# Kernel tuning notes

Hardware: AMD Instinct MI355X
Metric: run time of the kernel (lower is better)

## Reference

```python
import jax, jax.numpy as jnp
import numpy as np
from jax import lax

KS = [3, 5, 7, 9]
DS = [1, 2, 3, 4]
BN_EPS = 1e-5


def setup_inputs() -> dict:
    key = jax.random.key(0)
    ks = jax.random.split(key, 16)
    B, Cin, H, W = 16, 64, 256, 256
    Ce = 64  # out_channels // 2
    inp = {"x": jax.random.normal(ks[0], (B, Cin, H, W), jnp.float32)}
    for i, (k, _) in enumerate(zip(KS, DS)):
        fan_in = Cin * k * k
        inp[f"w{i}"] = jax.random.normal(ks[1 + i], (Ce, Cin, k, k), jnp.float32) / np.sqrt(fan_in)
        inp[f"b{i}"] = jnp.zeros((Ce,), jnp.float32)
    inp["bn_scale"] = jnp.ones((4, Ce), jnp.float32)
    inp["bn_bias"] = jnp.zeros((4, Ce), jnp.float32)
    inp["bn_mean"] = jax.random.normal(ks[5], (4, Ce), jnp.float32) * 0.1
    inp["bn_var"] = jax.random.uniform(ks[6], (4, Ce), jnp.float32, 0.5, 1.5)
    inp["gate_w"] = jax.random.normal(ks[7], (4, Cin), jnp.float32) / np.sqrt(Cin)
    inp["gate_b"] = jnp.zeros((4,), jnp.float32)
    return inp


def _expert(x, w, b, scale, bias, mean, var, k, d):
    pad = d * (k - 1) // 2
    y = lax.conv_general_dilated(
        x, w, window_strides=(2, 2), padding=[(pad, pad), (pad, pad)],
        rhs_dilation=(d, d), dimension_numbers=("NCHW", "OIHW", "NCHW"))
    y = y + b[None, :, None, None]
    inv = scale * lax.rsqrt(var + BN_EPS)
    y = y * inv[None, :, None, None] + (bias - mean * inv)[None, :, None, None]
    return jax.nn.gelu(y, approximate=False)


def reference(x, w0, b0, w1, b1, w2, b2, w3, b3,
              bn_scale, bn_bias, bn_mean, bn_var, gate_w, gate_b):
    B = x.shape[0]
    # Gate: global average pool -> linear -> softmax -> top-2 renormalized
    pooled = x.mean(axis=(2, 3))                    # (B, Cin)
    gates = jax.nn.softmax(pooled @ gate_w.T + gate_b, axis=1)  # (B, 4)
    top2_w, top2_idx = lax.top_k(gates, 2)
    top2_w = top2_w / (top2_w.sum(axis=1, keepdims=True) + 1e-8)
    # Dense compute of all 4 experts (faithful to original module)
    ws, bs = [w0, w1, w2, w3], [b0, b1, b2, b3]
    outs = [
        _expert(x, ws[i], bs[i], bn_scale[i], bn_bias[i], bn_mean[i], bn_var[i], KS[i], DS[i])
        for i in range(4)
    ]
    E = jnp.stack(outs, axis=1)                     # (B, 4, Ce, H/2, W/2)
    sel = jnp.take_along_axis(E, top2_idx[:, :, None, None, None], axis=1)  # (B,2,Ce,h,w)
    weighted = sel * top2_w[:, :, None, None, None]
    # concat top-2 along channel dim == reshape (B,2,Ce,h,w) -> (B,2*Ce,h,w)
    Bc, two, Ce, h, w = weighted.shape
    return weighted.reshape(Bc, two * Ce, h, w)
```

## Files before the change

kernel.cpp:

```cpp
#include <hip/hip_runtime.h>
#include <hip/hip_bf16.h>
#include <math.h>

#define CIN 64
#define CE  64
#define HH  256
#define WW  256
#define OHW 128
#define PW  288
#define PH  288
#define WOFF 19600
#define TOFF (WOFF + 6144)

typedef __attribute__((ext_vector_type(8))) short bf16x8;
typedef __attribute__((ext_vector_type(4))) float f32x4;

static __device__ __forceinline__ unsigned short f2bf(float f) {
    __hip_bfloat16 h = __float2bfloat16(f);
    return *reinterpret_cast<unsigned short*>(&h);
}

#define GLOAD16(gsrc, ldst)                                                        \
    __builtin_amdgcn_global_load_lds(                                              \
        (const __attribute__((address_space(1))) void*)(gsrc),                     \
        (__attribute__((address_space(3))) void*)(ldst), 16, 0, 0)

template <bool PRE>
__global__ __launch_bounds__(256)
void poolcvt_kernel(const float* __restrict__ x, unsigned short* __restrict__ xbf,
                    float* __restrict__ partial) {
    int blk = blockIdx.x;
    int rc = blockIdx.y;
    int tid = threadIdx.x, lane = tid & 63, wv = tid >> 6;
    int c0 = lane * 4;
    const float* xb = x + (size_t)blk * 8 * (HH * WW);
    unsigned short* pl = xbf + (size_t)blk * (PW * PH) * 8;
    float s[8];
#pragma unroll
    for (int j = 0; j < 8; ++j) s[j] = 0.f;
#pragma unroll 1
    for (int rr = wv; rr < 32; rr += 4) {
        int h = rc * 32 + rr;
        float4 v[8];
#pragma unroll
        for (int j = 0; j < 8; ++j)
            v[j] = *reinterpret_cast<const float4*>(xb + (size_t)j * (HH * WW) + h * WW + c0);
#pragma unroll
        for (int j = 0; j < 8; ++j) s[j] += (v[j].x + v[j].y) + (v[j].z + v[j].w);
        if (PRE) {
            size_t o16 = ((size_t)(16 + h) * PW + 16 + c0);
            unsigned short u[4][8];
#pragma unroll
            for (int j = 0; j < 8; ++j) {
                u[0][j] = f2bf(v[j].x);
                u[1][j] = f2bf(v[j].y);
                u[2][j] = f2bf(v[j].z);
                u[3][j] = f2bf(v[j].w);
            }
#pragma unroll
            for (int cc = 0; cc < 4; ++cc)
                *reinterpret_cast<bf16x8*>(pl + (o16 + cc) * 8) =
                    *reinterpret_cast<const bf16x8*>(u[cc]);
        }
    }
    if (PRE) {
        bf16x8 z = (bf16x8)(short)0;
#pragma unroll 1
        for (int i = tid; i < 32 * 32; i += 256) {
            int rr = i >> 5, cc = i & 31;
            int pr = 16 + rc * 32 + rr;
            int pc = (cc < 16) ? cc : (256 + cc);
            *reinterpret_cast<bf16x8*>(pl + ((size_t)pr * PW + pc) * 8) = z;
        }
        if (rc == 0) {
#pragma unroll 1
            for (int i = tid; i < 16 * PW; i += 256)
                *reinterpret_cast<bf16x8*>(pl + (size_t)i * 8) = z;
        }
        if (rc == 7) {
#pragma unroll 1
            for (int i = tid; i < 16 * PW; i += 256)
                *reinterpret_cast<bf16x8*>(pl + ((size_t)(272 * PW) + i) * 8) = z;
        }
    }
#pragma unroll
    for (int j = 0; j < 8; ++j) {
#pragma unroll
        for (int m = 32; m >= 1; m >>= 1) s[j] += __shfl_xor(s[j], m, 64);
    }
    __shared__ float red[4][8];
    if (lane == 0) {
#pragma unroll
        for (int j = 0; j < 8; ++j) red[wv][j] = s[j];
    }
    __syncthreads();
    if (tid < 8) {
        int j = tid;
        float t = (red[0][j] + red[1][j]) + (red[2][j] + red[3][j]);
        partial[(blk * 8 + rc) * 8 + j] = t;
    }
}

__global__ __launch_bounds__(64)
void gate_kernel(const float* __restrict__ partial, const float* __restrict__ gw,
                 const float* __restrict__ gb, int* __restrict__ sel_idx,
                 float* __restrict__ sel_w) {
    int b = blockIdx.x;
    int c = threadIdx.x;
    float p = 0.f;
#pragma unroll
    for (int rc = 0; rc < 8; ++rc)
        p += partial[(((b * 8 + (c >> 3)) * 8) + rc) * 8 + (c & 7)];
    p *= (1.0f / (HH * WW));
    float l[4];
#pragma unroll
    for (int e = 0; e < 4; ++e) l[e] = p * gw[e * CIN + c];
#pragma unroll
    for (int m = 32; m >= 1; m >>= 1) {
#pragma unroll
        for (int e = 0; e < 4; ++e) l[e] += __shfl_xor(l[e], m, 64);
    }
    if (c == 0) {
        float g[4], s = 0.f;
#pragma unroll
        for (int e = 0; e < 4; ++e) l[e] += gb[e];
        float mx = fmaxf(fmaxf(l[0], l[1]), fmaxf(l[2], l[3]));
#pragma unroll
        for (int e = 0; e < 4; ++e) { g[e] = expf(l[e] - mx); s += g[e]; }
#pragma unroll
        for (int e = 0; e < 4; ++e) g[e] /= s;
        int i1 = 0;
        for (int e = 1; e < 4; ++e) if (g[e] > g[i1]) i1 = e;
        int i2 = -1;
        for (int e = 0; e < 4; ++e) {
            if (e == i1) continue;
            if (i2 < 0 || g[e] > g[i2]) i2 = e;
        }
        float den = g[i1] + g[i2] + 1e-8f;
        sel_idx[b * 2 + 0] = i1;
        sel_idx[b * 2 + 1] = i2;
        sel_w[b * 2 + 0] = g[i1] / den;
        sel_w[b * 2 + 1] = g[i2] / den;
    }
}

__global__ void order_kernel(const int* __restrict__ sel_idx, int* __restrict__ ord) {
    if (threadIdx.x == 0) {
        int pos = 0;
        const int pri[4] = {3, 2, 1, 0};
        for (int pi = 0; pi < 4; ++pi)
            for (int bs = 0; bs < 32; ++bs)
                if (sel_idx[bs] == pri[pi]) ord[pos++] = bs;
    }
}

__global__ __launch_bounds__(256)
void bnprep_kernel(const float* __restrict__ b0, const float* __restrict__ b1,
                   const float* __restrict__ b2, const float* __restrict__ b3,
                   const float* __restrict__ bns, const float* __restrict__ bnb,
                   const float* __restrict__ bnm, const float* __restrict__ bnv,
                   float2* __restrict__ cbn) {
    int i = threadIdx.x;
    int e = i >> 6, co = i & 63;
    const float* be = (e == 0) ? b0 : (e == 1) ? b1 : (e == 2) ? b2 : b3;
    float inv = bns[i] * rsqrtf(bnv[i] + 1e-5f);
    float beta = bnb[i] - bnm[i] * inv + be[co] * inv;
    cbn[i] = make_float2(inv, beta);
}

__global__ __launch_bounds__(256)
void wprep_all_kernel(const float* __restrict__ w0, const float* __restrict__ w1,
                      const float* __restrict__ w2, const float* __restrict__ w3,
                      unsigned short* __restrict__ wq) {
    int cb = blockIdx.x;
    int y = blockIdx.y;
    const float* w;
    int g0, k, GE;
    size_t base;
    if (y < 3)       { w = w0; g0 = y;      k = 3; GE = 3;  base = 0; }
    else if (y < 10) { w = w1; g0 = y - 3;  k = 5; GE = 7;  base = 49152; }
    else if (y < 23) { w = w2; g0 = y - 10; k = 7; GE = 13; base = 163840; }
    else             { w = w3; g0 = y - 23; k = 9; GE = 21; base = 376832; }
    int k2 = k * k;
    int t = threadIdx.x, tl = t >> 6, co = t & 63;
    int tap = g0 * 4 + tl;
    unsigned short vals[8];
#pragma unroll
    for (int j = 0; j < 8; ++j) {
        float v = 0.f;
        if (tap < k2) v = w[(size_t)(co * CIN + cb * 8 + j) * k2 + tap];
        vals[j] = f2bf(v);
    }
    *reinterpret_cast<bf16x8*>(&wq[base + (size_t)(cb * GE + g0) * 2048 + t * 8]) =
        *reinterpret_cast<const bf16x8*>(vals);
}

template <int K, int D, int GE, bool EVEN, bool PRE>
__device__ __forceinline__ void conv_body(const float* __restrict__ xb,
                                          const unsigned short* __restrict__ xpb,
                                          const unsigned short* __restrict__ wq,
                                          unsigned short* __restrict__ lds,
                                          f32x4 acc[4][4],
                                          int ih0, int iw0, int lane, int wv, int tid) {
    constexpr int K2 = K * K;
    constexpr int TS = 31 + (K - 1) * D;
    constexpr int S = (TS + 1) / 2;
    constexpr int HPW = S * 8;
    constexpr int PITCH = 2 * HPW;
    constexpr int NRC = (TS + 1) / 2;
    constexpr int NEL = EVEN ? NRC * NRC : TS * 2 * S;
    constexpr int ITER = (NEL + 255) / 256;
    constexpr int DH = EVEN ? D / 2 : 0;
    constexpr size_t PLANE = (size_t)PW * PH * 8;
    constexpr int RSTEP = EVEN ? NRC * 16 : PITCH * 4;
    int p = lane & 15, hi = lane >> 4;

    if constexpr (PRE) {
        int gofs[ITER];
#pragma unroll
        for (int i = 0; i < ITER; ++i) {
            int idx = tid + i * 256;
            if (idx > NEL - 1) idx = NEL - 1;
            int ih, iw;
            if constexpr (EVEN) {
                int r = idx / NRC, c = idx - r * NRC;
                ih = ih0 + 16 + 2 * r;
                iw = iw0 + 16 + 2 * c;
            } else {
                int r = idx / (2 * S), rem = idx - r * (2 * S);
                int half = rem >= S ? 1 : 0;
                int sl = rem - half * S;
                int c = 2 * sl + half;
                if (c > TS - 1) c = TS - 1;
                ih = ih0 + 16 + r;
                iw = iw0 + 16 + c;
            }
            gofs[i] = (ih * PW + iw) * 8;
        }
        if (tid < 4 * GE) {
            int tapc = tid < K2 ? tid : K2 - 1;
            int kh = tapc / K, kw = tapc % K;
            int off;
            if constexpr (EVEN)
                off = (DH * kh * NRC + DH * kw) * 16;
            else
                off = D * kh * PITCH * 2 + (kw & 1) * HPW * 2 +
                      (((D * kw) - (kw & 1)) >> 1) * 16;
            *reinterpret_cast<int*>(&lds[TOFF + tid * 2]) = off;
        }
        __syncthreads();
        const int* tab = reinterpret_cast<const int*>(&lds[TOFF]);
        const char* ldsc = reinterpret_cast<const char*>(lds);
        int baseB = EVEN ? ((wv * 4 * NRC + p) * 16) : (wv * 16 * PITCH + p * 16);

#pragma unroll 1
        for (int cb = 0; cb < 8; ++cb) {
            __builtin_amdgcn_s_barrier();
            const unsigned short* xp = xpb + (size_t)cb * PLANE;
#pragma unroll
            for (int i = 0; i < ITER; ++i) {
                if (tid + i * 256 < NEL)
                    GLOAD16(xp + gofs[i], &lds[(tid + i * 256) * 8]);
            }
            const unsigned short* wcb = wq + (size_t)cb * GE * 2048;
            GLOAD16(wcb + tid * 8, &lds[WOFF + tid * 8]);
            GLOAD16(wcb + 2048 + tid * 8, &lds[WOFF + 2048 + tid * 8]);
            int toffCur = tab[hi];
#pragma unroll
            for (int g = 0; g < GE; ++g) {
                if (g == GE - 1) asm volatile("s_waitcnt vmcnt(0)" ::: "memory");
                else             asm volatile("s_waitcnt vmcnt(1)" ::: "memory");
                __builtin_amdgcn_s_barrier();
                if (g + 2 < GE)
                    GLOAD16(wcb + (size_t)(g + 2) * 2048 + tid * 8,
                            &lds[WOFF + ((g + 2) % 3) * 2048 + tid * 8]);
                int toffNext = (g + 1 < GE) ? tab[(g + 1) * 4 + hi] : 0;
                const unsigned short* wl = &lds[WOFF + (g % 3) * 2048 + hi * 512 + p * 8];
                bf16x8 a0 = *reinterpret_cast<const bf16x8*>(wl);
                bf16x8 a1 = *reinterpret_cast<const bf16x8*>(wl + 128);
                bf16x8 a2 = *reinterpret_cast<const bf16x8*>(wl + 256);
                bf16x8 a3 = *reinterpret_cast<const bf16x8*>(wl + 384);
                const char* bp = ldsc + (baseB + toffCur);
#pragma unroll
                for (int j = 0; j < 4; ++j) {
                    const bf16x8 bf = *reinterpret_cast<const bf16x8*>(bp + j * RSTEP);
                    acc[j][0] = __builtin_amdgcn_mfma_f32_16x16x32_bf16(a0, bf, acc[j][0], 0, 0, 0);
                    acc[j][1] = __builtin_amdgcn_mfma_f32_16x16x32_bf16(a1, bf, acc[j][1], 0, 0, 0);
                    acc[j][2] = __builtin_amdgcn_mfma_f32_16x16x32_bf16(a2, bf, acc[j][2], 0, 0, 0);
                    acc[j][3] = __builtin_amdgcn_mfma_f32_16x16x32_bf16(a3, bf, acc[j][3], 0, 0, 0);
                }
                toffCur = toffNext;
            }
        }
    } else {
#pragma unroll 1
        for (int cb = 0; cb < 8; ++cb) {
            __syncthreads();
            const float* xc8 = xb + (size_t)cb * 8 * (HH * WW);
#pragma unroll 1
            for (int idx = tid; idx < NEL; idx += 256) {
                int ih, iw;
                if constexpr (EVEN) {
                    int r = idx / NRC, c = idx - r * NRC;
                    ih = ih0 + 2 * r; iw = iw0 + 2 * c;
                } else {
                    int r = idx / (2 * S), rem = idx - r * (2 * S);
                    int half = rem >= S ? 1 : 0;
                    int sl = rem - half * S;
                    int c = min(2 * sl + half, TS - 1);
                    ih = ih0 + r; iw = iw0 + c;
                }
                int ihc = min(max(ih, 0), HH - 1), iwc = min(max(iw, 0), WW - 1);
                bool ok = ((unsigned)ih < (unsigned)HH) && ((unsigned)iw < (unsigned)WW);
                unsigned short u[8];
                const float* src = xc8 + ihc * WW + iwc;
#pragma unroll
                for (int j = 0; j < 8; ++j) u[j] = f2bf(ok ? src[(size_t)j * (HH * WW)] : 0.f);
                *reinterpret_cast<bf16x8*>(&lds[idx * 8]) = *reinterpret_cast<const bf16x8*>(u);
            }
            __syncthreads();
            const unsigned short* wcb = wq + (size_t)cb * GE * 2048;
#pragma unroll 2
            for (int g = 0; g < GE; ++g) {
                int tap = g * 4 + hi;
                int tapc = tap < K2 ? tap : K2 - 1;
                int kh = tapc / K, kw = tapc % K;
                const unsigned short* wg = wcb + g * 2048 + hi * 512;
                bf16x8 a0 = *reinterpret_cast<const bf16x8*>(wg + p * 8);
                bf16x8 a1 = *reinterpret_cast<const bf16x8*>(wg + 128 + p * 8);
                bf16x8 a2 = *reinterpret_cast<const bf16x8*>(wg + 256 + p * 8);
                bf16x8 a3 = *reinterpret_cast<const bf16x8*>(wg + 384 + p * 8);
                if constexpr (EVEN) {
                    int ec = p + (D / 2) * kw;
                    int erb = wv * 4 + (D / 2) * kh;
#pragma unroll
                    for (int j = 0; j < 4; ++j) {
                        const bf16x8 bf = *reinterpret_cast<const bf16x8*>(
                            &lds[((erb + j) * NRC + ec) * 8]);
                        acc[j][0] = __builtin_amdgcn_mfma_f32_16x16x32_bf16(a0, bf, acc[j][0], 0, 0, 0);
                        acc[j][1] = __builtin_amdgcn_mfma_f32_16x16x32_bf16(a1, bf, acc[j][1], 0, 0, 0);
                        acc[j][2] = __builtin_amdgcn_mfma_f32_16x16x32_bf16(a2, bf, acc[j][2], 0, 0, 0);
                        acc[j][3] = __builtin_amdgcn_mfma_f32_16x16x32_bf16(a3, bf, acc[j][3], 0, 0, 0);
                    }
                } else {
                    int ic = 2 * p + D * kw;
                    int bbase = (ic & 1) * HPW + (ic >> 1) * 8;
                    int irb = D * kh + wv * 8;
#pragma unroll
                    for (int j = 0; j < 4; ++j) {
                        const bf16x8 bf = *reinterpret_cast<const bf16x8*>(
                            &lds[(irb + 2 * j) * PITCH + bbase]);
                        acc[j][0] = __builtin_amdgcn_mfma_f32_16x16x32_bf16(a0, bf, acc[j][0], 0, 0, 0);
                        acc[j][1] = __builtin_amdgcn_mfma_f32_16x16x32_bf16(a1, bf, acc[j][1], 0, 0, 0);
                        acc[j][2] = __builtin_amdgcn_mfma_f32_16x16x32_bf16(a2, bf, acc[j][2], 0, 0, 0);
                        acc[j][3] = __builtin_amdgcn_mfma_f32_16x16x32_bf16(a3, bf, acc[j][3], 0, 0, 0);
                    }
                }
            }
        }
    }
}

template <bool PRE>
__global__ __launch_bounds__(256, 3)
void conv_moe_kernel(const float* __restrict__ x, const unsigned short* __restrict__ xbf,
                     const unsigned short* __restrict__ wq,
                     const float2* __restrict__ cbn,
                     const int* __restrict__ sel_idx, const float* __restrict__ sel_w,
                     const int* __restrict__ ord, float* __restrict__ out) {
    __shared__ __align__(16) unsigned short lds[TOFF + 176];

    int bidx = blockIdx.x;
    int bs = ord[bidx >> 6];
    int tile = bidx & 63;
    int b = bs >> 1, slot = bs & 1;
    int e = sel_idx[bs];
    float gwt = sel_w[bs];
    int oh0 = (tile >> 3) * 16, ow0 = (tile & 7) * 16;
    const float* xb = x + (size_t)b * CIN * HH * WW;
    const unsigned short* xpb = xbf + (size_t)b * 8 * (PW * PH) * 8;
    int tid = threadIdx.x, lane = tid & 63, wv = tid >> 6;
    int p = lane & 15, hi = lane >> 4;

    f32x4 acc[4][4];
#pragma unroll
    for (int j = 0; j < 4; ++j)
#pragma unroll
        for (int ct = 0; ct < 4; ++ct) acc[j][ct] = (f32x4){0.f, 0.f, 0.f, 0.f};

    switch (e) {
        case 0:
            conv_body<3, 1, 3, false, PRE>(xb, xpb, wq, lds, acc, oh0 * 2 - 1, ow0 * 2 - 1, lane, wv, tid);
            break;
        case 1:
            conv_body<5, 2, 7, true, PRE>(xb, xpb, wq + 49152, lds, acc, oh0 * 2 - 4, ow0 * 2 - 4, lane, wv, tid);
            break;
        case 2:
            conv_body<7, 3, 13, false, PRE>(xb, xpb, wq + 163840, lds, acc, oh0 * 2 - 9, ow0 * 2 - 9, lane, wv, tid);
            break;
        default:
            conv_body<9, 4, 21, true, PRE>(xb, xpb, wq + 376832, lds, acc, oh0 * 2 - 16, ow0 * 2 - 16, lane, wv, tid);
            break;
    }

    float* ob = out + (size_t)(b * 128 + slot * 64) * (OHW * OHW);
#pragma unroll
    for (int ct = 0; ct < 4; ++ct) {
#pragma unroll
        for (int reg = 0; reg < 4; ++reg) {
            int co = ct * 16 + hi * 4 + reg;
            float2 cb2 = cbn[e * CE + co];
#pragma unroll
            for (int j = 0; j < 4; ++j) {
                float y = acc[j][ct][reg] * cb2.x + cb2.y;
                float u = y * (1.5957691216f + 0.0714295766f * y * y);
                float gl = y / (1.0f + __expf(-u));
                int oh = oh0 + wv * 4 + j, ow = ow0 + p;
                ob[(size_t)co * (OHW * OHW) + oh * OHW + ow] = gl * gwt;
            }
        }
    }
}

extern "C" void kernel_launch(void* const* d_in, const int* in_sizes, int n_in,
                              void* d_out, int out_size, void* d_ws, size_t ws_size,
                              hipStream_t stream) {
    const float* x   = (const float*)d_in[0];
    const float* w0  = (const float*)d_in[1];
    const float* b0  = (const float*)d_in[2];
    const float* w1  = (const float*)d_in[3];
    const float* b1  = (const float*)d_in[4];
    const float* w2  = (const float*)d_in[5];
    const float* b2  = (const float*)d_in[6];
    const float* w3  = (const float*)d_in[7];
    const float* b3  = (const float*)d_in[8];
    const float* bns = (const float*)d_in[9];
    const float* bnb = (const float*)d_in[10];
    const float* bnm = (const float*)d_in[11];
    const float* bnv = (const float*)d_in[12];
    const float* gw  = (const float*)d_in[13];
    const float* gb  = (const float*)d_in[14];
    float* out = (float*)d_out;

    char* ws = (char*)d_ws;
    float* partial = (float*)ws;
    int* sel_idx   = (int*)(ws + 32768);
    float* sel_w   = (float*)(ws + 32896);
    int* ord       = (int*)(ws + 33024);
    float2* cbn    = (float2*)(ws + 33280);
    unsigned short* wq = (unsigned short*)(ws + 40960);
    unsigned short* xbf = (unsigned short*)(ws + 2097152);
    const size_t NEED = 2097152ull + (size_t)128 * PW * PH * 16;
    bool pre = ws_size >= NEED;

    if (pre) poolcvt_kernel<true><<<dim3(128, 8), 256, 0, stream>>>(x, xbf, partial);
    else     poolcvt_kernel<false><<<dim3(128, 8), 256, 0, stream>>>(x, xbf, partial);
    gate_kernel<<<dim3(16), 64, 0, stream>>>(partial, gw, gb, sel_idx, sel_w);
    order_kernel<<<dim3(1), 64, 0, stream>>>(sel_idx, ord);
    bnprep_kernel<<<dim3(1), 256, 0, stream>>>(b0, b1, b2, b3, bns, bnb, bnm, bnv, cbn);
    wprep_all_kernel<<<dim3(8, 44), 256, 0, stream>>>(w0, w1, w2, w3, wq);

    if (pre)
        conv_moe_kernel<true><<<dim3(2048), 256, 0, stream>>>(
            x, xbf, wq, cbn, sel_idx, sel_w, ord, out);
    else
        conv_moe_kernel<false><<<dim3(2048), 256, 0, stream>>>(
            x, xbf, wq, cbn, sel_idx, sel_w, ord, out);
}
```

Before: 259.3 us.

## Widen conv output tile to 16x32 with 512-thread blocks sharing weights

Each conv block now covers a 16x32 output tile using 8 waves (512 threads) instead of 16x16 with 4 waves. The input halo and the per-group weight slices staged in LDS are shared by twice as many outputs, so halo re-reads and weight loads per output drop. Only the lower half of the threads issue weight loads. LDS moves to dynamic shared memory of about 75 KB, and the launch bounds change, which may cut the number of resident blocks per CU. The pipelining waitcnt logic is changed to match the uneven number of outstanding loads per thread.

New measurement: 273.8 us. 1.06x slower.

```diff
diff --git a/kernel.cpp b/kernel.cpp
--- a/kernel.cpp
+++ b/kernel.cpp
@@ -9,8 +9,9 @@
 #define OHW 128
 #define PW  288
 #define PH  288
-#define WOFF 19600
+#define WOFF 32144
 #define TOFF (WOFF + 6144)
+#define SHMEM 76928
 
 typedef __attribute__((ext_vector_type(8))) short bf16x8;
 typedef __attribute__((ext_vector_type(4))) float f32x4;
@@ -203,27 +204,29 @@
                                           f32x4 acc[4][4],
                                           int ih0, int iw0, int lane, int wv, int tid) {
     constexpr int K2 = K * K;
-    constexpr int TS = 31 + (K - 1) * D;
-    constexpr int S = (TS + 1) / 2;
+    constexpr int TS_H = 31 + (K - 1) * D;
+    constexpr int TS_W = 63 + (K - 1) * D;
+    constexpr int S = (TS_W + 1) / 2;
     constexpr int HPW = S * 8;
     constexpr int PITCH = 2 * HPW;
-    constexpr int NRC = (TS + 1) / 2;
-    constexpr int NEL = EVEN ? NRC * NRC : TS * 2 * S;
-    constexpr int ITER = (NEL + 255) / 256;
+    constexpr int NRH = (TS_H + 1) / 2, NRW = (TS_W + 1) / 2;
+    constexpr int NEL = EVEN ? NRH * NRW : TS_H * 2 * S;
+    constexpr int ITER = (NEL + 511) / 512;
     constexpr int DH = EVEN ? D / 2 : 0;
     constexpr size_t PLANE = (size_t)PW * PH * 8;
-    constexpr int RSTEP = EVEN ? NRC * 16 : PITCH * 4;
+    constexpr int RSTEP = EVEN ? NRW * 16 : PITCH * 4;
     int p = lane & 15, hi = lane >> 4;
+    int wv2 = wv & 3, wh = wv >> 2;
 
     if constexpr (PRE) {
         int gofs[ITER];
 #pragma unroll
         for (int i = 0; i < ITER; ++i) {
-            int idx = tid + i * 256;
+            int idx = tid + i * 512;
             if (idx > NEL - 1) idx = NEL - 1;
             int ih, iw;
             if constexpr (EVEN) {
-                int r = idx / NRC, c = idx - r * NRC;
+                int r = idx / NRW, c = idx - r * NRW;
                 ih = ih0 + 16 + 2 * r;
                 iw = iw0 + 16 + 2 * c;
             } else {
@@ -231,7 +234,7 @@
                 int half = rem >= S ? 1 : 0;
                 int sl = rem - half * S;
                 int c = 2 * sl + half;
-                if (c > TS - 1) c = TS - 1;
+                if (c > TS_W - 1) c = TS_W - 1;
                 ih = ih0 + 16 + r;
                 iw = iw0 + 16 + c;
             }
@@ -242,7 +245,7 @@
             int kh = tapc / K, kw = tapc % K;
             int off;
             if constexpr (EVEN)
-                off = (DH * kh * NRC + DH * kw) * 16;
+                off = (DH * kh * NRW + DH * kw) * 16;
             else
                 off = D * kh * PITCH * 2 + (kw & 1) * HPW * 2 +
                       (((D * kw) - (kw & 1)) >> 1) * 16;
@@ -251,7 +254,9 @@
         __syncthreads();
         const int* tab = reinterpret_cast<const int*>(&lds[TOFF]);
         const char* ldsc = reinterpret_cast<const char*>(lds);
-        int baseB = EVEN ? ((wv * 4 * NRC + p) * 16) : (wv * 16 * PITCH + p * 16);
+        int baseB = EVEN ? ((wv2 * 4 * NRW + p + 16 * wh) * 16)
+                         : (wv2 * 16 * PITCH + (p + 16 * wh) * 16);
+        bool lowhalf = tid < 256;
 
 #pragma unroll 1
         for (int cb = 0; cb < 8; ++cb) {
@@ -259,19 +264,27 @@
             const unsigned short* xp = xpb + (size_t)cb * PLANE;
 #pragma unroll
             for (int i = 0; i < ITER; ++i) {
-                if (tid + i * 256 < NEL)
-                    GLOAD16(xp + gofs[i], &lds[(tid + i * 256) * 8]);
+                if (tid + i * 512 < NEL)
+                    GLOAD16(xp + gofs[i], &lds[(tid + i * 512) * 8]);
             }
             const unsigned short* wcb = wq + (size_t)cb * GE * 2048;
-            GLOAD16(wcb + tid * 8, &lds[WOFF + tid * 8]);
-            GLOAD16(wcb + 2048 + tid * 8, &lds[WOFF + 2048 + tid * 8]);
+            if (lowhalf) {
+                GLOAD16(wcb + tid * 8, &lds[WOFF + tid * 8]);
+                GLOAD16(wcb + 2048 + tid * 8, &lds[WOFF + 2048 + tid * 8]);
+            }
             int toffCur = tab[hi];
 #pragma unroll
             for (int g = 0; g < GE; ++g) {
-                if (g == GE - 1) asm volatile("s_waitcnt vmcnt(0)" ::: "memory");
-                else             asm volatile("s_waitcnt vmcnt(1)" ::: "memory");
+                if (g == GE - 1) {
+                    asm volatile("s_waitcnt vmcnt(0)" ::: "memory");
+                } else if (g == 0) {
+                    if (lowhalf) asm volatile("s_waitcnt vmcnt(1)" ::: "memory");
+                    else         asm volatile("s_waitcnt vmcnt(0)" ::: "memory");
+                } else {
+                    asm volatile("s_waitcnt vmcnt(1)" ::: "memory");
+                }
                 __builtin_amdgcn_s_barrier();
-                if (g + 2 < GE)
+                if (g + 2 < GE && lowhalf)
                     GLOAD16(wcb + (size_t)(g + 2) * 2048 + tid * 8,
                             &lds[WOFF + ((g + 2) % 3) * 2048 + tid * 8]);
                 int toffNext = (g + 1 < GE) ? tab[(g + 1) * 4 + hi] : 0;
@@ -298,16 +311,16 @@
             __syncthreads();
             const float* xc8 = xb + (size_t)cb * 8 * (HH * WW);
 #pragma unroll 1
-            for (int idx = tid; idx < NEL; idx += 256) {
+            for (int idx = tid; idx < NEL; idx += 512) {
                 int ih, iw;
                 if constexpr (EVEN) {
-                    int r = idx / NRC, c = idx - r * NRC;
+                    int r = idx / NRW, c = idx - r * NRW;
                     ih = ih0 + 2 * r; iw = iw0 + 2 * c;
                 } else {
                     int r = idx / (2 * S), rem = idx - r * (2 * S);
                     int half = rem >= S ? 1 : 0;
                     int sl = rem - half * S;
-                    int c = min(2 * sl + half, TS - 1);
+                    int c = min(2 * sl + half, TS_W - 1);
                     ih = ih0 + r; iw = iw0 + c;
                 }
                 int ihc = min(max(ih, 0), HH - 1), iwc = min(max(iw, 0), WW - 1);
@@ -330,31 +343,24 @@
                 bf16x8 a1 = *reinterpret_cast<const bf16x8*>(wg + 128 + p * 8);
                 bf16x8 a2 = *reinterpret_cast<const bf16x8*>(wg + 256 + p * 8);
                 bf16x8 a3 = *reinterpret_cast<const bf16x8*>(wg + 384 + p * 8);
-                if constexpr (EVEN) {
-                    int ec = p + (D / 2) * kw;
-                    int erb = wv * 4 + (D / 2) * kh;
-#pragma unroll
-                    for (int j = 0; j < 4; ++j) {
-                        const bf16x8 bf = *reinterpret_cast<const bf16x8*>(
-                            &lds[((erb + j) * NRC + ec) * 8]);
-                        acc[j][0] = __builtin_amdgcn_mfma_f32_16x16x32_bf16(a0, bf, acc[j][0], 0, 0, 0);
-                        acc[j][1] = __builtin_amdgcn_mfma_f32_16x16x32_bf16(a1, bf, acc[j][1], 0, 0, 0);
-                        acc[j][2] = __builtin_amdgcn_mfma_f32_16x16x32_bf16(a2, bf, acc[j][2], 0, 0, 0);
-                        acc[j][3] = __builtin_amdgcn_mfma_f32_16x16x32_bf16(a3, bf, acc[j][3], 0, 0, 0);
+#pragma unroll
+                for (int j = 0; j < 4; ++j) {
+                    const bf16x8* bfp;
+                    if constexpr (EVEN) {
+                        int ec = p + 16 * wh + (D / 2) * kw;
+                        int erb = wv2 * 4 + (D / 2) * kh + j;
+                        bfp = reinterpret_cast<const bf16x8*>(&lds[(erb * NRW + ec) * 8]);
+                    } else {
+                        int ic = 2 * (p + 16 * wh) + D * kw;
+                        int bbase = (ic & 1) * HPW + (ic >> 1) * 8;
+                        int irb = D * kh + wv2 * 8 + 2 * j;
+                        bfp = reinterpret_cast<const bf16x8*>(&lds[irb * PITCH + bbase]);
                     }
-                } else {
-                    int ic = 2 * p + D * kw;
-                    int bbase = (ic & 1) * HPW + (ic >> 1) * 8;
-                    int irb = D * kh + wv * 8;
-#pragma unroll
-                    for (int j = 0; j < 4; ++j) {
-                        const bf16x8 bf = *reinterpret_cast<const bf16x8*>(
-                            &lds[(irb + 2 * j) * PITCH + bbase]);
-                        acc[j][0] = __builtin_amdgcn_mfma_f32_16x16x32_bf16(a0, bf, acc[j][0], 0, 0, 0);
-                        acc[j][1] = __builtin_amdgcn_mfma_f32_16x16x32_bf16(a1, bf, acc[j][1], 0, 0, 0);
-                        acc[j][2] = __builtin_amdgcn_mfma_f32_16x16x32_bf16(a2, bf, acc[j][2], 0, 0, 0);
-                        acc[j][3] = __builtin_amdgcn_mfma_f32_16x16x32_bf16(a3, bf, acc[j][3], 0, 0, 0);
-                    }
+                    const bf16x8 bf = *bfp;
+                    acc[j][0] = __builtin_amdgcn_mfma_f32_16x16x32_bf16(a0, bf, acc[j][0], 0, 0, 0);
+                    acc[j][1] = __builtin_amdgcn_mfma_f32_16x16x32_bf16(a1, bf, acc[j][1], 0, 0, 0);
+                    acc[j][2] = __builtin_amdgcn_mfma_f32_16x16x32_bf16(a2, bf, acc[j][2], 0, 0, 0);
+                    acc[j][3] = __builtin_amdgcn_mfma_f32_16x16x32_bf16(a3, bf, acc[j][3], 0, 0, 0);
                 }
             }
         }
@@ -362,25 +368,26 @@
 }
 
 template <bool PRE>
-__global__ __launch_bounds__(256, 3)
+__global__ __launch_bounds__(512, 4)
 void conv_moe_kernel(const float* __restrict__ x, const unsigned short* __restrict__ xbf,
                      const unsigned short* __restrict__ wq,
                      const float2* __restrict__ cbn,
                      const int* __restrict__ sel_idx, const float* __restrict__ sel_w,
                      const int* __restrict__ ord, float* __restrict__ out) {
-    __shared__ __align__(16) unsigned short lds[TOFF + 176];
+    extern __shared__ __align__(16) unsigned short lds[];
 
     int bidx = blockIdx.x;
-    int bs = ord[bidx >> 6];
-    int tile = bidx & 63;
+    int bs = ord[bidx >> 5];
+    int tile = bidx & 31;
     int b = bs >> 1, slot = bs & 1;
     int e = sel_idx[bs];
     float gwt = sel_w[bs];
-    int oh0 = (tile >> 3) * 16, ow0 = (tile & 7) * 16;
+    int oh0 = (tile >> 2) * 16, ow0 = (tile & 3) * 32;
     const float* xb = x + (size_t)b * CIN * HH * WW;
     const unsigned short* xpb = xbf + (size_t)b * 8 * (PW * PH) * 8;
     int tid = threadIdx.x, lane = tid & 63, wv = tid >> 6;
     int p = lane & 15, hi = lane >> 4;
+    int wv2 = wv & 3, wh = wv >> 2;
 
     f32x4 acc[4][4];
 #pragma unroll
@@ -415,7 +422,7 @@
                 float y = acc[j][ct][reg] * cb2.x + cb2.y;
                 float u = y * (1.5957691216f + 0.0714295766f * y * y);
                 float gl = y / (1.0f + __expf(-u));
-                int oh = oh0 + wv * 4 + j, ow = ow0 + p;
+                int oh = oh0 + wv2 * 4 + j, ow = ow0 + wh * 16 + p;
                 ob[(size_t)co * (OHW * OHW) + oh * OHW + ow] = gl * gwt;
             }
         }
@@ -453,6 +460,11 @@
     const size_t NEED = 2097152ull + (size_t)128 * PW * PH * 16;
     bool pre = ws_size >= NEED;
 
+    hipFuncSetAttribute(reinterpret_cast<const void*>(&conv_moe_kernel<true>),
+                        hipFuncAttributeMaxDynamicSharedMemorySize, SHMEM);
+    hipFuncSetAttribute(reinterpret_cast<const void*>(&conv_moe_kernel<false>),
+                        hipFuncAttributeMaxDynamicSharedMemorySize, SHMEM);
+
     if (pre) poolcvt_kernel<true><<<dim3(128, 8), 256, 0, stream>>>(x, xbf, partial);
     else     poolcvt_kernel<false><<<dim3(128, 8), 256, 0, stream>>>(x, xbf, partial);
     gate_kernel<<<dim3(16), 64, 0, stream>>>(partial, gw, gb, sel_idx, sel_w);
@@ -461,9 +473,9 @@
     wprep_all_kernel<<<dim3(8, 44), 256, 0, stream>>>(w0, w1, w2, w3, wq);
 
     if (pre)
-        conv_moe_kernel<true><<<dim3(2048), 256, 0, stream>>>(
+        conv_moe_kernel<true><<<dim3(1024), 512, SHMEM, stream>>>(
             x, xbf, wq, cbn, sel_idx, sel_w, ord, out);
     else
-        conv_moe_kernel<false><<<dim3(2048), 256, 0, stream>>>(
+        conv_moe_kernel<false><<<dim3(1024), 512, SHMEM, stream>>>(
             x, xbf, wq, cbn, sel_idx, sel_w, ord, out);
 }
```
